# Performance work log

Measured on AMD Instinct MI355X. Metric: run time of the kernel, lower is better.

## Reference

```python
import jax, jax.numpy as jnp
import numpy as np

N_NODES = 50000


def setup_inputs() -> dict:
    key = jax.random.key(0)
    k1, k2, k3, k4, k5 = jax.random.split(key, 5)
    x = jax.random.normal(k1, (50000, 256), dtype=jnp.float32)
    edge_rows = jax.random.randint(k2, (1600000,), 0, N_NODES, dtype=jnp.int32)
    edge_cols = jax.random.randint(k3, (1600000,), 0, N_NODES, dtype=jnp.int32)
    edge_vals = jax.random.uniform(k4, (1600000,), dtype=jnp.float32)
    W = jax.random.normal(k5, (256, 128), dtype=jnp.float32) * (6.0 / (256 + 128)) ** 0.5  # glorot scale
    b = jnp.zeros((128,), dtype=jnp.float32)
    return {"x": x, "edge_rows": edge_rows, "edge_cols": edge_cols,
            "edge_vals": edge_vals, "W": W, "b": b}


def reference(x, edge_rows, edge_cols, edge_vals, W, b):
    # pre_sup = x @ W   -> [N, output_dim]
    pre_sup = jnp.matmul(x, W)
    # SpMM: output[r] = sum_{edges e with row r} val_e * pre_sup[col_e]
    msgs = edge_vals[:, None] * pre_sup[edge_cols]          # [E, output_dim]
    output = jax.ops.segment_sum(msgs, edge_rows, num_segments=N_NODES)
    output = output + b
    return jax.nn.relu(output)
```

## Files before the change

kernel.cpp:

```cpp
#include <hip/hip_runtime.h>

#define K_DIM 256
#define OD 128
#define BSH 5
#define BROWS 32
#define BCAP 2048
#define FILL_CHUNK 4096
#define NB_MAX 2048

typedef __attribute__((ext_vector_type(8))) short short8;
typedef __attribute__((ext_vector_type(4))) float f32x4;

__device__ inline unsigned short f2bf(float f) {
    unsigned u = __float_as_uint(f);
    unsigned r = (u + 0x7fffu + ((u >> 16) & 1u)) >> 16;
    return (unsigned short)r;
}

union Frag8 { short8 s; uint4 u; };

__global__ __launch_bounds__(256) void init_pack(const float* __restrict__ W,
                                                 uint4* __restrict__ wb,
                                                 int* __restrict__ gcur, int NB) {
    if ((int)blockIdx.x == 16) {
        for (int i = threadIdx.x; i < NB; i += 256) gcur[i * 16] = i * BCAP;
        return;
    }
    int t = blockIdx.x * 256 + threadIdx.x;
    if (t >= 8 * 8 * 64) return;
    int l  = t & 63;
    int n  = (t >> 6) & 7;
    int ks = t >> 9;
    int g  = l >> 4;
    int col = 16 * n + (l & 15);
    int kb  = 32 * ks + 4 * g;
    unsigned short e[8];
    #pragma unroll
    for (int j = 0; j < 8; ++j) {
        int k = kb + (j & 3) + 16 * (j >> 2);
        e[j] = f2bf(W[(size_t)k * OD + col]);
    }
    uint4 u;
    u.x = (unsigned)e[0] | ((unsigned)e[1] << 16);
    u.y = (unsigned)e[2] | ((unsigned)e[3] << 16);
    u.z = (unsigned)e[4] | ((unsigned)e[5] << 16);
    u.w = (unsigned)e[6] | ((unsigned)e[7] << 16);
    wb[t] = u;
}

__global__ __launch_bounds__(512) void gemm_fill(const float* __restrict__ x,
                                                 const uint4* __restrict__ wb,
                                                 unsigned* __restrict__ prebp,
                                                 const int* __restrict__ rows,
                                                 const int* __restrict__ cols,
                                                 const float* __restrict__ vals,
                                                 int* __restrict__ gcur,
                                                 uint2* __restrict__ csr,
                                                 int M, int E, int NB, int nGemm) {
    __shared__ int cnt[NB_MAX];
    __shared__ int base[NB_MAX];
    const int t = threadIdx.x;

    if ((int)blockIdx.x >= nGemm) {
        const int e0 = ((int)blockIdx.x - nGemm) * FILL_CHUNK;
        for (int i = t; i < NB; i += 512) cnt[i] = 0;
        __syncthreads();
        int r[8]; int c[8]; float v[8];
        #pragma unroll
        for (int it = 0; it < 8; ++it) {
            int i = e0 + it * 512 + t;
            if (i < E) {
                r[it] = rows[i]; c[it] = cols[i]; v[it] = vals[i];
                atomicAdd(&cnt[r[it] >> BSH], 1);
            } else r[it] = -1;
        }
        __syncthreads();
        for (int bkt = t; bkt < NB; bkt += 512) {
            int cn = cnt[bkt];
            base[bkt] = cn ? atomicAdd(&gcur[bkt * 16], cn) : 0;
        }
        __syncthreads();
        #pragma unroll
        for (int it = 0; it < 8; ++it) {
            if (r[it] >= 0) {
                int pos = atomicAdd(&base[r[it] >> BSH], 1);
                csr[pos] = make_uint2(((unsigned)(r[it] & (BROWS - 1)) << 16) | (unsigned)c[it],
                                      __float_as_uint(v[it]));
            }
        }
        return;
    }

    const int l = t & 63;
    const int w = t >> 6;
    const int g = l >> 4;
    const int row  = blockIdx.x * 128 + w * 16 + (l & 15);
    const int rowc = row < M ? row : M - 1;
    const float* xp = x + (size_t)rowc * K_DIM + g * 4;

    f32x4 acc[8];
    #pragma unroll
    for (int n = 0; n < 8; ++n) acc[n] = (f32x4){0.f, 0.f, 0.f, 0.f};

    #pragma unroll
    for (int ks = 0; ks < 8; ++ks) {
        float4 xa = *reinterpret_cast<const float4*>(xp + 32 * ks);
        float4 xb = *reinterpret_cast<const float4*>(xp + 32 * ks + 16);
        Frag8 a;
        a.u.x = (unsigned)f2bf(xa.x) | ((unsigned)f2bf(xa.y) << 16);
        a.u.y = (unsigned)f2bf(xa.z) | ((unsigned)f2bf(xa.w) << 16);
        a.u.z = (unsigned)f2bf(xb.x) | ((unsigned)f2bf(xb.y) << 16);
        a.u.w = (unsigned)f2bf(xb.z) | ((unsigned)f2bf(xb.w) << 16);
        const uint4* wp = wb + (size_t)ks * 8 * 64 + l;
        #pragma unroll
        for (int n = 0; n < 8; ++n) {
            Frag8 bfrag;
            bfrag.u = wp[n * 64];
            acc[n] = __builtin_amdgcn_mfma_f32_16x16x32_bf16(a.s, bfrag.s, acc[n], 0, 0, 0);
        }
    }
    const int rbase = blockIdx.x * 128 + w * 16 + g * 4;
    #pragma unroll
    for (int r = 0; r < 4; ++r) {
        int ro = rbase + r;
        if (ro < M) {
            unsigned* dst = prebp + (size_t)ro * 64 + (l & 15);
            #pragma unroll
            for (int m = 0; m < 4; ++m)
                dst[16 * m] = (unsigned)f2bf(acc[m][r]) |
                              ((unsigned)f2bf(acc[m + 4][r]) << 16);
        }
    }
}

__global__ __launch_bounds__(512) void gather_sort(const int* __restrict__ gcur,
                                                   const uint2* __restrict__ csr,
                                                   const unsigned* __restrict__ prebp,
                                                   const float* __restrict__ b,
                                                   float* __restrict__ out, int M) {
    __shared__ uint2 sbuf[BCAP];
    __shared__ int cnt[BROWS];
    __shared__ int beg[BROWS];
    __shared__ int ofs[BROWS];
    const int t   = threadIdx.x;
    const int bkt = (int)blockIdx.x;
    int nE = gcur[bkt * 16] - bkt * BCAP;
    nE = nE < BCAP ? nE : BCAP;
    const uint2* ep = csr + (size_t)bkt * BCAP;

    if (t < BROWS) cnt[t] = 0;
    __syncthreads();
    uint2 er[4];
    #pragma unroll
    for (int k = 0; k < 4; ++k) {
        int i = t + k * 512;
        if (i < nE) {
            er[k] = ep[i];
            atomicAdd(&cnt[er[k].x >> 16], 1);
        } else er[k].x = 0xffffffffu;
    }
    __syncthreads();
    if (t < 64) {
        int c  = (t < BROWS) ? cnt[t] : 0;
        int sc = c;
        #pragma unroll
        for (int o = 1; o < 32; o <<= 1) {
            int u = __shfl_up(sc, o, 64);
            if ((t & 63) >= o) sc += u;
        }
        if (t < BROWS) { beg[t] = sc - c; ofs[t] = sc - c; }
    }
    __syncthreads();
    #pragma unroll
    for (int k = 0; k < 4; ++k) {
        if (er[k].x != 0xffffffffu) {
            int r   = (int)(er[k].x >> 16);
            int pos = atomicAdd(&ofs[r], 1);
            sbuf[pos] = make_uint2(er[k].x & 0xffffu, er[k].y);
        }
    }
    __syncthreads();

    const int l = t & 63, w = t >> 6;
    const float bv0 = b[l], bv1 = b[64 + l];
    const unsigned* pl = prebp + l;
    #pragma unroll 1
    for (int q = 0; q < 4; ++q) {
        int rr = w + 8 * q;
        int r  = (bkt << BSH) + rr;
        if (r >= M) continue;
        int j  = beg[rr];
        int je = j + cnt[rr];
        float a0 = 0.f, a1 = 0.f;
        for (; j + 7 < je; j += 8) {
            uint2 e0 = sbuf[j],     e1 = sbuf[j + 1], e2 = sbuf[j + 2], e3 = sbuf[j + 3];
            uint2 e4 = sbuf[j + 4], e5 = sbuf[j + 5], e6 = sbuf[j + 6], e7 = sbuf[j + 7];
            unsigned p0 = pl[(size_t)e0.x * 64];
            unsigned p1 = pl[(size_t)e1.x * 64];
            unsigned p2 = pl[(size_t)e2.x * 64];
            unsigned p3 = pl[(size_t)e3.x * 64];
            unsigned p4 = pl[(size_t)e4.x * 64];
            unsigned p5 = pl[(size_t)e5.x * 64];
            unsigned p6 = pl[(size_t)e6.x * 64];
            unsigned p7 = pl[(size_t)e7.x * 64];
            float v0 = __uint_as_float(e0.y), v1 = __uint_as_float(e1.y);
            float v2 = __uint_as_float(e2.y), v3 = __uint_as_float(e3.y);
            float v4 = __uint_as_float(e4.y), v5 = __uint_as_float(e5.y);
            float v6 = __uint_as_float(e6.y), v7 = __uint_as_float(e7.y);
            a0 = fmaf(v0, __uint_as_float(p0 << 16), a0);
            a1 = fmaf(v0, __uint_as_float(p0 & 0xffff0000u), a1);
            a0 = fmaf(v1, __uint_as_float(p1 << 16), a0);
            a1 = fmaf(v1, __uint_as_float(p1 & 0xffff0000u), a1);
            a0 = fmaf(v2, __uint_as_float(p2 << 16), a0);
            a1 = fmaf(v2, __uint_as_float(p2 & 0xffff0000u), a1);
            a0 = fmaf(v3, __uint_as_float(p3 << 16), a0);
            a1 = fmaf(v3, __uint_as_float(p3 & 0xffff0000u), a1);
            a0 = fmaf(v4, __uint_as_float(p4 << 16), a0);
            a1 = fmaf(v4, __uint_as_float(p4 & 0xffff0000u), a1);
            a0 = fmaf(v5, __uint_as_float(p5 << 16), a0);
            a1 = fmaf(v5, __uint_as_float(p5 & 0xffff0000u), a1);
            a0 = fmaf(v6, __uint_as_float(p6 << 16), a0);
            a1 = fmaf(v6, __uint_as_float(p6 & 0xffff0000u), a1);
            a0 = fmaf(v7, __uint_as_float(p7 << 16), a0);
            a1 = fmaf(v7, __uint_as_float(p7 & 0xffff0000u), a1);
        }
        for (; j < je; ++j) {
            uint2 e = sbuf[j];
            unsigned p = pl[(size_t)e.x * 64];
            float v = __uint_as_float(e.y);
            a0 = fmaf(v, __uint_as_float(p << 16), a0);
            a1 = fmaf(v, __uint_as_float(p & 0xffff0000u), a1);
        }
        out[(size_t)r * OD + l]      = fmaxf(a0 + bv0, 0.f);
        out[(size_t)r * OD + 64 + l] = fmaxf(a1 + bv1, 0.f);
    }
}

__global__ __launch_bounds__(256) void spmm_scatter(const int* __restrict__ rows,
                                                    const int* __restrict__ cols,
                                                    const float* __restrict__ vals,
                                                    const unsigned* __restrict__ prebp,
                                                    float* __restrict__ out, int E) {
    const int e    = (int)((blockIdx.x * 256u + threadIdx.x) >> 6);
    const int lane = threadIdx.x & 63;
    if (e >= E) return;
    const int   r = rows[e];
    const int   c = cols[e];
    const float v = vals[e];
    unsigned p = prebp[(size_t)c * 64 + lane];
    float* o = out + (size_t)r * OD;
    unsafeAtomicAdd(o + lane,      v * __uint_as_float(p << 16));
    unsafeAtomicAdd(o + lane + 64, v * __uint_as_float(p & 0xffff0000u));
}

__global__ __launch_bounds__(256) void bias_relu(float* __restrict__ out,
                                                 const float* __restrict__ b, int n4) {
    int i = blockIdx.x * 256 + threadIdx.x;
    if (i >= n4) return;
    float4 v = reinterpret_cast<float4*>(out)[i];
    int c = (i & ((OD / 4) - 1)) << 2;
    float4 bv = *reinterpret_cast<const float4*>(b + c);
    v.x = fmaxf(v.x + bv.x, 0.f);
    v.y = fmaxf(v.y + bv.y, 0.f);
    v.z = fmaxf(v.z + bv.z, 0.f);
    v.w = fmaxf(v.w + bv.w, 0.f);
    reinterpret_cast<float4*>(out)[i] = v;
}

extern "C" void kernel_launch(void* const* d_in, const int* in_sizes, int n_in,
                              void* d_out, int out_size, void* d_ws, size_t ws_size,
                              hipStream_t stream) {
    const float* x     = (const float*)d_in[0];
    const int*   erows = (const int*)d_in[1];
    const int*   ecols = (const int*)d_in[2];
    const float* evals = (const float*)d_in[3];
    const float* W     = (const float*)d_in[4];
    const float* b     = (const float*)d_in[5];
    float*       out   = (float*)d_out;

    const int M  = in_sizes[0] / K_DIM;
    const int E  = in_sizes[1];
    const int NB = (M + BROWS - 1) >> BSH;

    char* ws = (char*)d_ws;
    size_t off = 0;
    auto alloc = [&](size_t bytes) { char* p = ws + off; off = (off + bytes + 15) & ~(size_t)15; return p; };
    unsigned* prebp = (unsigned*)alloc((size_t)M * 64 * sizeof(unsigned));
    uint4*    wb    = (uint4*)alloc((size_t)8 * 8 * 64 * sizeof(uint4));
    int*      gcur  = (int*)  alloc((size_t)NB * 16 * sizeof(int));
    uint2*    csr   = (uint2*)alloc((size_t)NB * BCAP * sizeof(uint2));
    const bool bucket_ok = (off <= ws_size) && (NB <= NB_MAX) && (M <= 65536);

    const int nGemm = (M + 127) / 128;
    const int nFill = (E + FILL_CHUNK - 1) / FILL_CHUNK;

    if (bucket_ok) {
        init_pack<<<17, 256, 0, stream>>>(W, wb, gcur, NB);
        gemm_fill<<<nGemm + nFill, 512, 0, stream>>>(x, wb, prebp, erows, ecols, evals,
                                                     gcur, csr, M, E, NB, nGemm);
        gather_sort<<<NB, 512, 0, stream>>>(gcur, csr, prebp, b, out, M);
    } else {
        init_pack<<<16, 256, 0, stream>>>(W, wb, gcur, 0);
        gemm_fill<<<nGemm, 512, 0, stream>>>(x, wb, prebp, nullptr, nullptr, nullptr,
                                             nullptr, nullptr, M, 0, 0, nGemm);
        hipMemsetAsync(d_out, 0, (size_t)out_size * sizeof(float), stream);
        spmm_scatter<<<(E + 3) / 4, 256, 0, stream>>>(erows, ecols, evals, prebp, out, E);
        bias_relu<<<(out_size / 4 + 255) / 256, 256, 0, stream>>>(out, b, out_size / 4);
    }
}
```

Before: 119.6 us.

## Split fused GEMM+bucket-fill kernel into separate GEMM and fill launches

Pulls the edge-bucketing fill work out of the combined GEMM/fill kernel into its own 1024-thread kernel, which runs after a standalone MFMA GEMM kernel on the same stream. The GEMM kernel shrinks to 256 threads and 64 rows per block and no longer reserves 16KB of shared memory for bucket counters, which may raise occupancy. In exchange the GEMM and fill phases no longer overlap inside one launch, and the extra kernel launch adds a serialization point.

```diff
diff --git a/kernel.cpp b/kernel.cpp
--- a/kernel.cpp
+++ b/kernel.cpp
@@ -5,6 +5,7 @@
 #define BSH 5
 #define BROWS 32
 #define BCAP 2048
+#define FILL_THREADS 1024
 #define FILL_CHUNK 4096
 #define NB_MAX 2048
 
@@ -48,53 +49,14 @@
     wb[t] = u;
 }
 
-__global__ __launch_bounds__(512) void gemm_fill(const float* __restrict__ x,
+__global__ __launch_bounds__(256) void gemm_mfma(const float* __restrict__ x,
                                                  const uint4* __restrict__ wb,
-                                                 unsigned* __restrict__ prebp,
-                                                 const int* __restrict__ rows,
-                                                 const int* __restrict__ cols,
-                                                 const float* __restrict__ vals,
-                                                 int* __restrict__ gcur,
-                                                 uint2* __restrict__ csr,
-                                                 int M, int E, int NB, int nGemm) {
-    __shared__ int cnt[NB_MAX];
-    __shared__ int base[NB_MAX];
+                                                 unsigned* __restrict__ prebp, int M) {
     const int t = threadIdx.x;
-
-    if ((int)blockIdx.x >= nGemm) {
-        const int e0 = ((int)blockIdx.x - nGemm) * FILL_CHUNK;
-        for (int i = t; i < NB; i += 512) cnt[i] = 0;
-        __syncthreads();
-        int r[8]; int c[8]; float v[8];
-        #pragma unroll
-        for (int it = 0; it < 8; ++it) {
-            int i = e0 + it * 512 + t;
-            if (i < E) {
-                r[it] = rows[i]; c[it] = cols[i]; v[it] = vals[i];
-                atomicAdd(&cnt[r[it] >> BSH], 1);
-            } else r[it] = -1;
-        }
-        __syncthreads();
-        for (int bkt = t; bkt < NB; bkt += 512) {
-            int cn = cnt[bkt];
-            base[bkt] = cn ? atomicAdd(&gcur[bkt * 16], cn) : 0;
-        }
-        __syncthreads();
-        #pragma unroll
-        for (int it = 0; it < 8; ++it) {
-            if (r[it] >= 0) {
-                int pos = atomicAdd(&base[r[it] >> BSH], 1);
-                csr[pos] = make_uint2(((unsigned)(r[it] & (BROWS - 1)) << 16) | (unsigned)c[it],
-                                      __float_as_uint(v[it]));
-            }
-        }
-        return;
-    }
-
     const int l = t & 63;
     const int w = t >> 6;
     const int g = l >> 4;
-    const int row  = blockIdx.x * 128 + w * 16 + (l & 15);
+    const int row  = blockIdx.x * 64 + w * 16 + (l & 15);
     const int rowc = row < M ? row : M - 1;
     const float* xp = x + (size_t)rowc * K_DIM + g * 4;
 
@@ -119,7 +81,7 @@
             acc[n] = __builtin_amdgcn_mfma_f32_16x16x32_bf16(a.s, bfrag.s, acc[n], 0, 0, 0);
         }
     }
-    const int rbase = blockIdx.x * 128 + w * 16 + g * 4;
+    const int rbase = blockIdx.x * 64 + w * 16 + g * 4;
     #pragma unroll
     for (int r = 0; r < 4; ++r) {
         int ro = rbase + r;
@@ -129,6 +91,45 @@
             for (int m = 0; m < 4; ++m)
                 dst[16 * m] = (unsigned)f2bf(acc[m][r]) |
                               ((unsigned)f2bf(acc[m + 4][r]) << 16);
+        }
+    }
+}
+
+__global__ __launch_bounds__(1024) void fill_bucket(const int* __restrict__ rows,
+                                                    const int* __restrict__ cols,
+                                                    const float* __restrict__ vals,
+                                                    int* __restrict__ gcur,
+                                                    uint2* __restrict__ csr, int E, int NB) {
+    __shared__ int cnt[NB_MAX];
+    __shared__ int base[NB_MAX];
+    const int t  = threadIdx.x;
+    const int e0 = blockIdx.x * FILL_CHUNK;
+    for (int i = t; i < NB; i += FILL_THREADS) cnt[i] = 0;
+    __syncthreads();
+    int  r[4]; int c[4]; float v[4]; bool ok[4];
+    #pragma unroll
+    for (int it = 0; it < 4; ++it) {
+        int i = e0 + it * FILL_THREADS + t;
+        ok[it] = (i < E);
+        if (ok[it]) {
+            r[it] = rows[i];
+            c[it] = cols[i];
+            v[it] = vals[i];
+            atomicAdd(&cnt[r[it] >> BSH], 1);
+        }
+    }
+    __syncthreads();
+    for (int bkt = t; bkt < NB; bkt += FILL_THREADS) {
+        int cn = cnt[bkt];
+        base[bkt] = cn ? atomicAdd(&gcur[bkt * 16], cn) : 0;
+    }
+    __syncthreads();
+    #pragma unroll
+    for (int it = 0; it < 4; ++it) {
+        if (ok[it]) {
+            int pos = atomicAdd(&base[r[it] >> BSH], 1);
+            csr[pos] = make_uint2(((unsigned)(r[it] & (BROWS - 1)) << 16) | (unsigned)c[it],
+                                  __float_as_uint(v[it]));
         }
     }
 }
@@ -291,18 +292,17 @@
     uint2*    csr   = (uint2*)alloc((size_t)NB * BCAP * sizeof(uint2));
     const bool bucket_ok = (off <= ws_size) && (NB <= NB_MAX) && (M <= 65536);
 
-    const int nGemm = (M + 127) / 128;
-    const int nFill = (E + FILL_CHUNK - 1) / FILL_CHUNK;
+    const int nGemm = (M + 63) / 64;
 
     if (bucket_ok) {
         init_pack<<<17, 256, 0, stream>>>(W, wb, gcur, NB);
-        gemm_fill<<<nGemm + nFill, 512, 0, stream>>>(x, wb, prebp, erows, ecols, evals,
-                                                     gcur, csr, M, E, NB, nGemm);
+        gemm_mfma<<<nGemm, 256, 0, stream>>>(x, wb, prebp, M);
+        fill_bucket<<<(E + FILL_CHUNK - 1) / FILL_CHUNK, FILL_THREADS, 0, stream>>>(
+            erows, ecols, evals, gcur, csr, E, NB);
         gather_sort<<<NB, 512, 0, stream>>>(gcur, csr, prebp, b, out, M);
     } else {
         init_pack<<<16, 256, 0, stream>>>(W, wb, gcur, 0);
-        gemm_fill<<<nGemm, 512, 0, stream>>>(x, wb, prebp, nullptr, nullptr, nullptr,
-                                             nullptr, nullptr, M, 0, 0, nGemm);
+        gemm_mfma<<<nGemm, 256, 0, stream>>>(x, wb, prebp, M);
         hipMemsetAsync(d_out, 0, (size_t)out_size * sizeof(float), stream);
         spmm_scatter<<<(E + 3) / 4, 256, 0, stream>>>(erows, ecols, evals, prebp, out, E);
         bias_relu<<<(out_size / 4 + 255) / 256, 256, 0, stream>>>(out, b, out_size / 4);
```

Measured after the change: 120.7 us. Within noise of the previous version (+0.9%).
